# Optimization experiments

Measured on AMD Instinct MI355X. Metric: run time of the kernel, lower is better.

The kernel has to match this reference:

```python
import jax, jax.numpy as jnp
import numpy as np

B, T, NX = 2, 2048, 512
H = 2                    # n_head (structurally forced to 2 by rns() broadcasting)
L = 64                   # num landmarks (cfg.MODEL.LANDMARK)
K = 32                   # rns neighbors per token
HD = NX // H // 2        # differential head dim = 128
EPS = 1e-5


def setup_inputs() -> dict:
    key = jax.random.key(0)
    ks = jax.random.split(key, 16)
    inp = {}
    inp["x"] = jax.random.normal(ks[0], (B, T, NX), jnp.float32)
    # linear weights (torch nn.Linear stores [out,in], applies x @ W.T)
    inp["wq"] = jax.random.normal(ks[1], (NX, NX), jnp.float32) * 0.02
    inp["wk"] = jax.random.normal(ks[2], (NX, NX), jnp.float32) * 0.02
    inp["wv"] = jax.random.normal(ks[3], (NX, NX), jnp.float32) * 0.02
    inp["wo"] = jax.random.normal(ks[4], (NX, NX), jnp.float32) * 0.02
    # landmark modulation params (kaiming-normal-ish init)
    inp["m1"] = jax.random.normal(ks[5], (2 * H, L, 1), jnp.float32)
    inp["m2"] = jax.random.normal(ks[6], (2 * H, 1, L), jnp.float32)
    # differential-attention lambda params
    inp["lq1"] = jax.random.normal(ks[7], (HD,), jnp.float32) * 0.1
    inp["lk1"] = jax.random.normal(ks[8], (HD,), jnp.float32) * 0.1
    inp["lq2"] = jax.random.normal(ks[9], (HD,), jnp.float32) * 0.1
    inp["lk2"] = jax.random.normal(ks[10], (HD,), jnp.float32) * 0.1
    inp["rms_g"] = jnp.ones((2 * HD,), jnp.float32)
    inp["l"] = 3  # layer depth for lambda_init_fn
    inp["num_landmark"] = L
    inp["rns_indices"] = jax.random.randint(ks[11], (B, T, K), 0, T)
    # random.sample(range(t), L) -> distinct indices
    inp["landmark"] = jax.random.permutation(ks[12], T)[:L]
    return inp


def _forward(x, wq, wk, wv, wo, m1, m2, lq1, lk1, lq2, lk2, rms_g,
             l, rns_indices, landmark):
    b, t, nx = x.shape
    hd = nx // H // 2
    q = x @ wq.T
    k = x @ wk.T
    v = x @ wv.T
    qh = q.reshape(b, t, 2 * H, hd).transpose(0, 2, 1, 3)   # [b,2H,t,hd]
    kh = k.reshape(b, t, 2 * H, hd).transpose(0, 2, 3, 1)   # [b,2H,hd,t]
    vh = v.reshape(b, t, H, 2 * hd).transpose(0, 2, 1, 3)   # [b,H,t,2hd]

    # landmark (Nystrom) low-rank factors, L2-normalized over head dim
    sq = qh[:, :, landmark, :]                               # [b,2H,L,hd]
    sk = kh[:, :, :, landmark]                               # [b,2H,hd,L]
    sq = sq / jnp.linalg.norm(sq, axis=3, keepdims=True)
    sk = sk / jnp.linalg.norm(sk, axis=2, keepdims=True)
    sq = m1[None] * sq
    sk = m2[None] * sk

    w1 = jnp.matmul(qh, sk)                                  # [b,2H,t,L]
    w2 = jnp.matmul(sq, kh)                                  # [b,2H,L,t]
    w = jnp.matmul(w1, w2)                                   # [b,2H,t,t]

    lam_init = 0.8 - 0.6 * np.exp(-0.3 * l)
    lam = jnp.exp(jnp.sum(lq1 * lk1)) - jnp.exp(jnp.sum(lq2 * lk2)) + lam_init

    # rns symmetric sparse mask: mask[b,i,j]=1 iff j in rns_indices[b,i] AND i in rns_indices[b,j]
    bi = jnp.arange(b)[:, None, None]
    ti = jnp.arange(t)[None, :, None]
    m = jnp.zeros((b, t, t), x.dtype).at[bi, ti, rns_indices].set(1.0)
    m = m * m.transpose(0, 2, 1)
    m4 = m[:, None]                                          # broadcast over heads

    p = jax.nn.softmax(w * m4 - 1e9 * (1.0 - m4), axis=-1)   # [b,2H,t,t]
    p5 = p.reshape(b, H, 2, t, t)
    # differential mixing (note: second term indexes the HEAD dim, requires H==2)
    wmix = (p5[:, :, 0] - lam * p5[:, :, 1]) + ((1.0 - lam) * p5[:, 1] - p5[:, 0])
    a = jnp.matmul(wmix, vh)                                 # [b,H,t,2hd]

    # RMSNorm sub-layer + (1 - lambda_init) scaling
    a = a * jax.lax.rsqrt(jnp.mean(a * a, axis=-1, keepdims=True) + EPS) * rms_g
    a = a * (1.0 - lam_init)
    return a.transpose(0, 2, 1, 3).reshape(b, t, H * 2 * hd) @ wo.T


def reference(x, wq, wk, wv, wo, m1, m2, lq1, lk1, lq2, lk2, rms_g,
              l, num_landmark, rns_indices, landmark):
    return _forward(x, wq, wk, wv, wo, m1, m2, lq1, lk1, lq2, lk2, rms_g,
                    l, rns_indices, landmark)
```

## Files before the change

### kernel.cpp

```cpp
#include <hip/hip_runtime.h>
#include <hip/hip_bf16.h>

#define BB 2
#define TT 2048
#define NX 512
#define NH 4
#define HD 128
#define LL 64
#define KK 32

typedef __bf16 bf16x8 __attribute__((ext_vector_type(8)));
typedef float f32x4 __attribute__((ext_vector_type(4)));
typedef unsigned short us;
typedef const unsigned int __attribute__((address_space(1)))* gptr_t;
typedef unsigned int __attribute__((address_space(3)))* lptr_t;

__device__ __forceinline__ us f2bf(float f) {
    unsigned u = __float_as_uint(f);
    unsigned r = (u + 0x7fffu + ((u >> 16) & 1u)) >> 16;
    return (us)r;
}
__device__ __forceinline__ float bf2f(us h) {
    return __uint_as_float(((unsigned)h) << 16);
}

__global__ void k_split_all(const float* __restrict__ x,
                            const float* __restrict__ wq, const float* __restrict__ wk,
                            const float* __restrict__ wv, const float* __restrict__ wo,
                            us* __restrict__ x_hi, us* __restrict__ x_lo,
                            us* __restrict__ wqkv_hi, us* __restrict__ wqkv_lo,
                            us* __restrict__ wo_hi, us* __restrict__ wo_lo,
                            const float* __restrict__ lq1, const float* __restrict__ lk1,
                            const float* __restrict__ lq2, const float* __restrict__ lk2,
                            const int* __restrict__ lint, float* __restrict__ scal,
                            float* __restrict__ cs)
{
    const int bidx = blockIdx.x;
    if (bidx == 3072) {
        const int tid = threadIdx.x;
        const f32x4 z = {0.f, 0.f, 0.f, 0.f};
        *reinterpret_cast<f32x4*>(cs + tid * 4) = z;
        if (tid < 64) {
            float s1 = lq1[tid] * lk1[tid] + lq1[tid + 64] * lk1[tid + 64];
            float s2 = lq2[tid] * lk2[tid] + lq2[tid + 64] * lk2[tid + 64];
            for (int off = 32; off; off >>= 1) { s1 += __shfl_xor(s1, off); s2 += __shfl_xor(s2, off); }
            if (tid == 0) {
                float lam_init = 0.8f - 0.6f * expf(-0.3f * (float)lint[0]);
                scal[0] = expf(s1) - expf(s2) + lam_init;
                scal[1] = lam_init;
            }
        }
        return;
    }
    const float* src;
    us* hi;
    us* lo;
    int pos;
    if (bidx < 2048) {
        src = x; hi = x_hi; lo = x_lo;
        pos = bidx * 1024 + threadIdx.x * 4;
    } else {
        const int w = (bidx - 2048) >> 8;
        const int p = (bidx - 2048) & 255;
        pos = p * 1024 + threadIdx.x * 4;
        if (w == 0)      { src = wq; hi = wqkv_hi;          lo = wqkv_lo; }
        else if (w == 1) { src = wk; hi = wqkv_hi + 262144; lo = wqkv_lo + 262144; }
        else if (w == 2) { src = wv; hi = wqkv_hi + 524288; lo = wqkv_lo + 524288; }
        else             { src = wo; hi = wo_hi;            lo = wo_lo; }
    }
    const float4 v = *reinterpret_cast<const float4*>(src + pos);
    ushort4 h, l;
    h.x = f2bf(v.x); l.x = f2bf(v.x - bf2f(h.x));
    h.y = f2bf(v.y); l.y = f2bf(v.y - bf2f(h.y));
    h.z = f2bf(v.z); l.z = f2bf(v.z - bf2f(h.z));
    h.w = f2bf(v.w); l.w = f2bf(v.w - bf2f(h.w));
    *reinterpret_cast<ushort4*>(hi + pos) = h;
    *reinterpret_cast<ushort4*>(lo + pos) = l;
}

template<int BN, int MODE>
__global__ __launch_bounds__(256) void k_gemm_big(
    const us* __restrict__ a_hi, const us* __restrict__ a_lo,
    const us* __restrict__ b_hi, const us* __restrict__ b_lo,
    us* __restrict__ vb, float* __restrict__ cout,
    us* __restrict__ qs_hi, us* __restrict__ qs_lo,
    us* __restrict__ ks_hi, us* __restrict__ ks_lo)
{
    constexpr int NB = BN / 32;
    __shared__ us lsA[64 * 64];
    __shared__ us lsB[BN * 64];
    const int tid = threadIdx.x;
    const int m0 = blockIdx.x * 64, n0 = blockIdx.y * BN;
    const int region = n0 >> 9;
    const int ncol0 = n0 & 511;
    const int l = tid & 63, wid = tid >> 6;
    const int wr = (wid >> 1) * 32, wc = (wid & 1) * (BN / 2);
    const int lr = l & 15;
    const int lkb = (l >> 4) * 16;
    f32x4 acc[2][NB] = {};

    const int r8 = tid >> 3;
    const int swzc8 = (((tid & 7) ^ (r8 & 7)) * 8);

    const int nstep = (MODE == 0) ? (region < 2 ? 24 : 16) : 8;
    for (int kt = 0; kt < nstep; ++kt) {
        const int seg = kt >> 3;
        const int koff = (kt & 7) * 64;
        const us* ab;
        const us* bb;
        if constexpr (MODE == 0) {
            if (region < 2) {
                ab = (seg < 2 ? a_hi : a_lo) + koff + swzc8;
                bb = (seg == 1 ? b_lo : b_hi) + koff + swzc8;
            } else {
                ab = (seg == 0 ? a_hi : a_lo) + koff + swzc8;
                bb = b_hi + koff + swzc8;
            }
        } else {
            ab = a_hi + koff + swzc8;
            bb = b_hi + koff + swzc8;
        }
        #pragma unroll
        for (int j = 0; j < 2; ++j)
            __builtin_amdgcn_global_load_lds((gptr_t)(ab + (size_t)(m0 + j * 32 + r8) * 512),
                                             (lptr_t)(lsA + j * 2048 + tid * 8), 16, 0, 0);
        #pragma unroll
        for (int j = 0; j < BN / 32; ++j)
            __builtin_amdgcn_global_load_lds((gptr_t)(bb + (size_t)(n0 + j * 32 + r8) * 512),
                                             (lptr_t)(lsB + j * 2048 + tid * 8), 16, 0, 0);
        __syncthreads();
        bf16x8 af[2][2], bfr[NB][2];
        #pragma unroll
        for (int m = 0; m < 2; ++m) {
            const int row = wr + m * 16 + lr;
            #pragma unroll
            for (int kk = 0; kk < 2; ++kk) {
                const int cb = (kk * 64 + lkb) ^ ((row & 7) << 4);
                af[m][kk] = *reinterpret_cast<const bf16x8*>(
                    (const char*)lsA + row * 128 + cb);
            }
        }
        #pragma unroll
        for (int n = 0; n < NB; ++n) {
            const int row = wc + n * 16 + lr;
            #pragma unroll
            for (int kk = 0; kk < 2; ++kk) {
                const int cb = (kk * 64 + lkb) ^ ((row & 7) << 4);
                bfr[n][kk] = *reinterpret_cast<const bf16x8*>(
                    (const char*)lsB + row * 128 + cb);
            }
        }
        #pragma unroll
        for (int kk = 0; kk < 2; ++kk)
            #pragma unroll
            for (int m = 0; m < 2; ++m)
                #pragma unroll
                for (int n = 0; n < NB; ++n)
                    acc[m][n] = __builtin_amdgcn_mfma_f32_16x16x32_bf16(
                        af[m][kk], bfr[n][kk], acc[m][n], 0, 0, 0);
        __syncthreads();
    }

    if constexpr (MODE == 0) {
        if (region < 2) {
            us* sh = (region == 0) ? qs_hi : ks_hi;
            us* slo = (region == 0) ? qs_lo : ks_lo;
            #pragma unroll
            for (int m = 0; m < 2; ++m) {
                const int row = m0 + wr + m * 16 + (l >> 4) * 4;
                #pragma unroll
                for (int n = 0; n < NB; ++n) {
                    const int col = ncol0 + wc + n * 16 + lr;
                    #pragma unroll
                    for (int r = 0; r < 4; ++r) {
                        const float val = acc[m][n][r];
                        const us h = f2bf(val);
                        sh[(size_t)(row + r) * 512 + col] = h;
                        slo[(size_t)(row + r) * 512 + col] = f2bf(val - bf2f(h));
                    }
                }
            }
        } else {
            #pragma unroll
            for (int m = 0; m < 2; ++m) {
                const int row = m0 + wr + m * 16 + (l >> 4) * 4;
                #pragma unroll
                for (int n = 0; n < NB; ++n) {
                    const int col = ncol0 + wc + n * 16 + lr;
                    #pragma unroll
                    for (int r = 0; r < 4; ++r)
                        vb[(size_t)(row + r) * 512 + col] = f2bf(acc[m][n][r]);
                }
            }
        }
    } else {
        #pragma unroll
        for (int m = 0; m < 2; ++m) {
            const int row = m0 + wr + m * 16 + (l >> 4) * 4;
            #pragma unroll
            for (int n = 0; n < NB; ++n) {
                const int col = n0 + wc + n * 16 + lr;
                #pragma unroll
                for (int r = 0; r < 4; ++r)
                    cout[(size_t)(row + r) * 512 + col] = acc[m][n][r];
            }
        }
    }
}

__global__ __launch_bounds__(256) void k_w12_colsum(
    const us* __restrict__ q_hi, const us* __restrict__ q_lo,
    const us* __restrict__ k_hi, const us* __restrict__ k_lo,
    const us* __restrict__ kn_hi, const us* __restrict__ kn_lo,
    const us* __restrict__ qn_hi, const us* __restrict__ qn_lo,
    float* __restrict__ w1, float* __restrict__ w2t,
    const us* __restrict__ vb, float* __restrict__ cs)
{
    const int blk = blockIdx.x;
    const int tid = threadIdx.x;
    if (blk >= 384) {
        const int c4 = tid * 4;
        const int b = c4 >> 9, c = c4 & 511;
        const int t0 = (blk - 384) * 64;
        const us* p = vb + ((size_t)(b * TT + t0)) * NX + c;
        f32x4 s = {0.f, 0.f, 0.f, 0.f};
        for (int t = 0; t < 64; ++t) {
            const ushort4 u = *reinterpret_cast<const ushort4*>(p + (size_t)t * NX);
            s[0] += bf2f(u.x); s[1] += bf2f(u.y); s[2] += bf2f(u.z); s[3] += bf2f(u.w);
        }
        atomicAdd(&cs[c4 + 0], s[0]);
        atomicAdd(&cs[c4 + 1], s[1]);
        atomicAdd(&cs[c4 + 2], s[2]);
        atomicAdd(&cs[c4 + 3], s[3]);
        return;
    }
    __shared__ us lsA[64 * 64];
    __shared__ us lsB[64 * 64];
    const int m0 = (blk & 31) * 64;
    const int y = (blk >> 5) % 6;
    const int z = blk / 192;
    const int hh = y % 3, b = y / 3;
    const int h = hh + 1;
    const us* ah = (z ? k_hi : q_hi) + ((size_t)b * 2048) * 512 + h * 128;
    const us* al = (z ? k_lo : q_lo) + ((size_t)b * 2048) * 512 + h * 128;
    const us* bhp = (z ? qn_hi : kn_hi) + (size_t)(b * 4 + h) * 64 * 128;
    const us* blp = (z ? qn_lo : kn_lo) + (size_t)(b * 4 + h) * 64 * 128;
    float* C = (z ? w2t : w1) + (size_t)(b * 3 + hh) * 2048 * 64;

    const int l = tid & 63, wid = tid >> 6;
    const int wr = (wid >> 1) * 32, wc = (wid & 1) * 32;
    const int lr = l & 15;
    const int lkb = (l >> 4) * 16;
    f32x4 acc[2][2] = {};
    const int r8 = tid >> 3;
    const int swzc8 = (((tid & 7) ^ (r8 & 7)) * 8);

    for (int kt = 0; kt < 6; ++kt) {
        const int seg = kt >> 1;
        const int koff = (kt & 1) * 64;
        const us* ab = (seg < 2 ? ah : al) + koff + swzc8;
        const us* bb = (seg == 1 ? blp : bhp) + koff + swzc8;
        #pragma unroll
        for (int j = 0; j < 2; ++j) {
            __builtin_amdgcn_global_load_lds((gptr_t)(ab + (size_t)(m0 + j * 32 + r8) * 512),
                                             (lptr_t)(lsA + j * 2048 + tid * 8), 16, 0, 0);
            __builtin_amdgcn_global_load_lds((gptr_t)(bb + (size_t)(j * 32 + r8) * 128),
                                             (lptr_t)(lsB + j * 2048 + tid * 8), 16, 0, 0);
        }
        __syncthreads();
        bf16x8 af[2][2], bfr[2][2];
        #pragma unroll
        for (int m = 0; m < 2; ++m) {
            const int row = wr + m * 16 + lr;
            #pragma unroll
            for (int kk = 0; kk < 2; ++kk) {
                const int cb = (kk * 64 + lkb) ^ ((row & 7) << 4);
                af[m][kk] = *reinterpret_cast<const bf16x8*>((const char*)lsA + row * 128 + cb);
            }
        }
        #pragma unroll
        for (int n = 0; n < 2; ++n) {
            const int row = wc + n * 16 + lr;
            #pragma unroll
            for (int kk = 0; kk < 2; ++kk) {
                const int cb = (kk * 64 + lkb) ^ ((row & 7) << 4);
                bfr[n][kk] = *reinterpret_cast<const bf16x8*>((const char*)lsB + row * 128 + cb);
            }
        }
        #pragma unroll
        for (int kk = 0; kk < 2; ++kk)
            #pragma unroll
            for (int m = 0; m < 2; ++m)
                #pragma unroll
                for (int n = 0; n < 2; ++n)
                    acc[m][n] = __builtin_amdgcn_mfma_f32_16x16x32_bf16(
                        af[m][kk], bfr[n][kk], acc[m][n], 0, 0, 0);
        __syncthreads();
    }

    #pragma unroll
    for (int m = 0; m < 2; ++m) {
        const int row = m0 + wr + m * 16 + (l >> 4) * 4;
        #pragma unroll
        for (int n = 0; n < 2; ++n) {
            const int col = wc + n * 16 + lr;
            #pragma unroll
            for (int r = 0; r < 4; ++r)
                C[(size_t)(row + r) * 64 + col] = acc[m][n][r];
        }
    }
}

__global__ __launch_bounds__(256) void k_norm_lm(
    const us* __restrict__ q_hi, const us* __restrict__ q_lo,
    const us* __restrict__ k_hi, const us* __restrict__ k_lo,
    const float* __restrict__ m1, const float* __restrict__ m2,
    const int* __restrict__ landmark,
    us* __restrict__ qn_hi, us* __restrict__ qn_lo,
    us* __restrict__ kn_hi, us* __restrict__ kn_lo)
{
    const int idx = blockIdx.x * 4 + (threadIdx.x >> 6);
    const int l = idx & 63;
    const int h = (idx >> 6) & 3;
    const int b = idx >> 8;
    const int lm = landmark[l];
    const int d = threadIdx.x & 63;

    const size_t qoff = ((size_t)(b * TT + lm)) * NX + h * HD;
    const float qa = bf2f(q_hi[qoff + d]) + bf2f(q_lo[qoff + d]);
    const float qb = bf2f(q_hi[qoff + d + 64]) + bf2f(q_lo[qoff + d + 64]);
    const float ka = bf2f(k_hi[qoff + d]) + bf2f(k_lo[qoff + d]);
    const float kb = bf2f(k_hi[qoff + d + 64]) + bf2f(k_lo[qoff + d + 64]);
    float sq = qa * qa + qb * qb;
    float sk = ka * ka + kb * kb;
    for (int off = 32; off; off >>= 1) { sq += __shfl_xor(sq, off); sk += __shfl_xor(sk, off); }
    const float invq = rsqrtf(sq) * m1[h * LL + l];
    const float invk = rsqrtf(sk) * m2[h * LL + l];
    const size_t base = (((size_t)(b * NH + h)) * LL + l) * HD;
    const float vq0 = qa * invq, vq1 = qb * invq;
    const float vk0 = ka * invk, vk1 = kb * invk;
    us h0;
    h0 = f2bf(vq0); qn_hi[base + d] = h0;      qn_lo[base + d] = f2bf(vq0 - bf2f(h0));
    h0 = f2bf(vq1); qn_hi[base + d + 64] = h0; qn_lo[base + d + 64] = f2bf(vq1 - bf2f(h0));
    h0 = f2bf(vk0); kn_hi[base + d] = h0;      kn_lo[base + d] = f2bf(vk0 - bf2f(h0));
    h0 = f2bf(vk1); kn_hi[base + d + 64] = h0; kn_lo[base + d + 64] = f2bf(vk1 - bf2f(h0));
}

__global__ __launch_bounds__(256) void k_sparse_attn(
    const float* __restrict__ w1, const float* __restrict__ w2t,
    const us* __restrict__ vb, const float* __restrict__ cs,
    const int* __restrict__ rns, const float* __restrict__ rms_g,
    const float* __restrict__ scal,
    us* __restrict__ ao)
{
    const int wid = threadIdx.x >> 6;
    const int lane = threadIdx.x & 63;
    const int bi = blockIdx.x * 4 + wid;
    const int b = bi >> 11, i = bi & 2047;

    __shared__ int   sl[4][32];
    __shared__ float plog[4][96];
    __shared__ float wmm[4][2][32];
    __shared__ float w1s[4][3][64];

    const int myidx = lane & 31;
    const int cand = rns[(size_t)bi * KK + myidx];
    int dup = 0;
    #pragma unroll
    for (int kk = 0; kk < 31; ++kk) {
        const int other = __shfl(cand, kk);
        dup |= (kk < myidx) & (other == cand);
    }
    const int* jrow = rns + ((size_t)(b * TT + cand)) * KK + (lane >> 5) * 16;
    int found = 0;
    #pragma unroll
    for (int kk = 0; kk < 16; ++kk) found |= (jrow[kk] == i);
    found |= __shfl_xor(found, 32);
    const int keep = (!dup) && found;
    const unsigned long long mask = __ballot(keep) & 0xffffffffull;
    const int sc = __popcll(mask);
    const int pos = __popcll(mask & ((1ull << myidx) - 1ull));
    if (lane < 32 && keep) sl[wid][pos] = cand;

    const float lam = scal[0], lam_init = scal[1];

    if (sc > 0) {
        #pragma unroll
        for (int r = 0; r < 3; ++r)
            w1s[wid][r][lane] = w1[(((size_t)(b * 3 + r)) * TT + i) * LL + lane];
        const int ntask = 3 * sc;
        for (int t0 = 0; t0 < ntask; t0 += 8) {
            const int t = t0 + (lane >> 3);
            float part = 0.f;
            if (t < ntask) {
                const int hh = t % 3, ss = t / 3;
                const int j = sl[wid][ss];
                const float* w2row = w2t + (((size_t)(b * 3 + hh)) * TT + j) * LL + (lane & 7) * 8;
                const float* w1p = &w1s[wid][hh][(lane & 7) * 8];
                #pragma unroll
                for (int e = 0; e < 8; ++e) part += w1p[e] * w2row[e];
            }
            part += __shfl_xor(part, 1);
            part += __shfl_xor(part, 2);
            part += __shfl_xor(part, 4);
            if (t < ntask && (lane & 7) == 0) plog[wid][t] = part;
        }
        if (lane < 3) {
            float mx = -1e30f;
            for (int ss = 0; ss < sc; ++ss) mx = fmaxf(mx, plog[wid][ss * 3 + lane]);
            float s = 0.f;
            for (int ss = 0; ss < sc; ++ss) {
                const float e = expf(plog[wid][ss * 3 + lane] - mx);
                plog[wid][ss * 3 + lane] = e;
                s += e;
            }
            const float inv = 1.0f / s;
            for (int ss = 0; ss < sc; ++ss) plog[wid][ss * 3 + lane] *= inv;
        }
        if (lane < sc) {
            const float p1 = plog[wid][lane * 3 + 0];
            const float p2 = plog[wid][lane * 3 + 1];
            const float p3 = plog[wid][lane * 3 + 2];
            wmm[wid][0][lane] = (1.0f - lam) * p2 - lam * p1;
            wmm[wid][1][lane] = p2 - p1 + (1.0f - 2.0f * lam) * p3;
        }
    }

    f32x4 acc0 = {0.f, 0.f, 0.f, 0.f}, acc1 = {0.f, 0.f, 0.f, 0.f};
    if (sc == 0) {
        const float cc = (1.0f - 2.0f * lam) * (1.0f / (float)TT);
        const f32x4 c0 = *reinterpret_cast<const f32x4*>(cs + b * NX + lane * 4);
        const f32x4 c1 = *reinterpret_cast<const f32x4*>(cs + b * NX + 256 + lane * 4);
        acc0 = cc * c0;
        acc1 = cc * c1;
    } else {
        for (int ss = 0; ss < sc; ++ss) {
            const float wa = wmm[wid][0][ss], wb = wmm[wid][1][ss];
            const us* vrow = vb + ((size_t)(b * TT + sl[wid][ss])) * NX;
            const ushort4 ua = *reinterpret_cast<const ushort4*>(vrow + lane * 4);
            const ushort4 ub = *reinterpret_cast<const ushort4*>(vrow + 256 + lane * 4);
            acc0[0] += wa * bf2f(ua.x); acc0[1] += wa * bf2f(ua.y);
            acc0[2] += wa * bf2f(ua.z); acc0[3] += wa * bf2f(ua.w);
            acc1[0] += wb * bf2f(ub.x); acc1[1] += wb * bf2f(ub.y);
            acc1[2] += wb * bf2f(ub.z); acc1[3] += wb * bf2f(ub.w);
        }
    }

    float s0 = acc0[0]*acc0[0] + acc0[1]*acc0[1] + acc0[2]*acc0[2] + acc0[3]*acc0[3];
    float s1 = acc1[0]*acc1[0] + acc1[1]*acc1[1] + acc1[2]*acc1[2] + acc1[3]*acc1[3];
    #pragma unroll
    for (int off = 32; off; off >>= 1) { s0 += __shfl_xor(s0, off); s1 += __shfl_xor(s1, off); }
    const float sc0 = rsqrtf(s0 * (1.0f / 256.0f) + 1e-5f);
    const float sc1 = rsqrtf(s1 * (1.0f / 256.0f) + 1e-5f);
    const float og = 1.0f - lam_init;
    const f32x4 g = *reinterpret_cast<const f32x4*>(rms_g + lane * 4);
    ushort4 h0, h1;
    #pragma unroll
    for (int e = 0; e < 4; ++e) {
        (&h0.x)[e] = f2bf(acc0[e] * sc0 * g[e] * og);
        (&h1.x)[e] = f2bf(acc1[e] * sc1 * g[e] * og);
    }
    *reinterpret_cast<ushort4*>(ao + (size_t)bi * NX + lane * 4) = h0;
    *reinterpret_cast<ushort4*>(ao + (size_t)bi * NX + 256 + lane * 4) = h1;
}

extern "C" void kernel_launch(void* const* d_in, const int* in_sizes, int n_in,
                              void* d_out, int out_size, void* d_ws, size_t ws_size,
                              hipStream_t stream)
{
    const float* x    = (const float*)d_in[0];
    const float* wq   = (const float*)d_in[1];
    const float* wk   = (const float*)d_in[2];
    const float* wv   = (const float*)d_in[3];
    const float* wo   = (const float*)d_in[4];
    const float* m1   = (const float*)d_in[5];
    const float* m2   = (const float*)d_in[6];
    const float* lq1  = (const float*)d_in[7];
    const float* lk1  = (const float*)d_in[8];
    const float* lq2  = (const float*)d_in[9];
    const float* lk2  = (const float*)d_in[10];
    const float* rmsg = (const float*)d_in[11];
    const int*   lint = (const int*)d_in[12];
    const int*   rns  = (const int*)d_in[14];
    const int*   lmk  = (const int*)d_in[15];
    float* out = (float*)d_out;
    float* ws  = (float*)d_ws;

    const size_t M2 = 2097152;
    const size_t W3 = 786432;
    float* w1   = ws;
    float* w2t  = ws + W3;
    float* cs   = ws + 2 * W3;
    float* scal = cs + 1024;
    us* S = (us*)(scal + 128);
    us* vb   = S;
    us* x_hi = S + M2;
    us* x_lo = S + 2 * M2;
    us* ao   = x_hi;
    us* q_hi = S + 3 * M2;
    us* q_lo = S + 4 * M2;
    us* k_hi = S + 5 * M2;
    us* k_lo = S + 6 * M2;
    us* wqkv_hi = S + 7 * M2;
    us* wqkv_lo = wqkv_hi + 786432;
    us* wo_hi = wqkv_lo + 786432;
    us* wo_lo = wo_hi + 262144;
    us* qn_hi = wo_lo + 262144;
    us* qn_lo = qn_hi + 65536;
    us* kn_hi = qn_lo + 65536;
    us* kn_lo = kn_hi + 65536;

    k_split_all<<<3073, 256, 0, stream>>>(x, wq, wk, wv, wo,
                                          x_hi, x_lo, wqkv_hi, wqkv_lo, wo_hi, wo_lo,
                                          lq1, lk1, lq2, lk2, lint, scal, cs);

    k_gemm_big<128, 0><<<dim3(64, 12), 256, 0, stream>>>(
        x_hi, x_lo, wqkv_hi, wqkv_lo, vb, nullptr, q_hi, q_lo, k_hi, k_lo);

    k_norm_lm<<<128, 256, 0, stream>>>(q_hi, q_lo, k_hi, k_lo, m1, m2, lmk,
                                       qn_hi, qn_lo, kn_hi, kn_lo);
    k_w12_colsum<<<416, 256, 0, stream>>>(q_hi, q_lo, k_hi, k_lo,
                                          kn_hi, kn_lo, qn_hi, qn_lo, w1, w2t, vb, cs);
    k_sparse_attn<<<1024, 256, 0, stream>>>(w1, w2t, vb, cs, rns, rmsg, scal, ao);

    k_gemm_big<64, 1><<<dim3(64, 8), 256, 0, stream>>>(
        ao, nullptr, wo_hi, nullptr, nullptr, out, nullptr, nullptr, nullptr, nullptr);
}
```

Measured before the change: 140.8 us.

## Precompute neighbor bitmap for mutual-membership test and shrink QKV GEMM tile

Builds a per-row T-bit bitmap of rns neighbors with atomicOr inside extra blocks of the split kernel, so the sparse attention kernel checks mutual membership with one bitmap load instead of scanning 32 indices of each candidate row. This replaces gather-heavy reads with a single word lookup. It adds a memset of the 1 MiB bitmap plus atomic traffic. Separately, the QKV GEMM tile changes from 128 to 64 with twice as many blocks, which raises parallelism.

```diff
diff --git a/kernel.cpp b/kernel.cpp
--- a/kernel.cpp
+++ b/kernel.cpp
@@ -33,9 +33,17 @@
                             const float* __restrict__ lq1, const float* __restrict__ lk1,
                             const float* __restrict__ lq2, const float* __restrict__ lk2,
                             const int* __restrict__ lint, float* __restrict__ scal,
-                            float* __restrict__ cs)
+                            float* __restrict__ cs,
+                            const int* __restrict__ rns, unsigned* __restrict__ bmap)
 {
     const int bidx = blockIdx.x;
+    if (bidx >= 3073) {
+        const int bi = (bidx - 3073) * 8 + (threadIdx.x >> 5);
+        const int lane = threadIdx.x & 31;
+        const int t = rns[(size_t)bi * KK + lane];
+        atomicOr(&bmap[(size_t)bi * 64 + (t >> 5)], 1u << (t & 31));
+        return;
+    }
     if (bidx == 3072) {
         const int tid = threadIdx.x;
         const f32x4 z = {0.f, 0.f, 0.f, 0.f};
@@ -349,8 +357,8 @@
 __global__ __launch_bounds__(256) void k_sparse_attn(
     const float* __restrict__ w1, const float* __restrict__ w2t,
     const us* __restrict__ vb, const float* __restrict__ cs,
-    const int* __restrict__ rns, const float* __restrict__ rms_g,
-    const float* __restrict__ scal,
+    const int* __restrict__ rns, const unsigned* __restrict__ bmap,
+    const float* __restrict__ rms_g, const float* __restrict__ scal,
     us* __restrict__ ao)
 {
     const int wid = threadIdx.x >> 6;
@@ -371,16 +379,12 @@
         const int other = __shfl(cand, kk);
         dup |= (kk < myidx) & (other == cand);
     }
-    const int* jrow = rns + ((size_t)(b * TT + cand)) * KK + (lane >> 5) * 16;
-    int found = 0;
-    #pragma unroll
-    for (int kk = 0; kk < 16; ++kk) found |= (jrow[kk] == i);
-    found |= __shfl_xor(found, 32);
-    const int keep = (!dup) && found;
+    const int found = (bmap[(size_t)(b * TT + cand) * 64 + (i >> 5)] >> (i & 31)) & 1;
+    const int keep = (lane < 32) && (!dup) && found;
     const unsigned long long mask = __ballot(keep) & 0xffffffffull;
     const int sc = __popcll(mask);
     const int pos = __popcll(mask & ((1ull << myidx) - 1ull));
-    if (lane < 32 && keep) sl[wid][pos] = cand;
+    if (keep) sl[wid][pos] = cand;
 
     const float lam = scal[0], lam_init = scal[1];
 
@@ -509,19 +513,22 @@
     us* qn_lo = qn_hi + 65536;
     us* kn_hi = qn_lo + 65536;
     us* kn_lo = kn_hi + 65536;
-
-    k_split_all<<<3073, 256, 0, stream>>>(x, wq, wk, wv, wo,
+    unsigned* bmap = (unsigned*)(kn_lo + 65536);
+
+    hipMemsetAsync(bmap, 0, 262144 * sizeof(unsigned), stream);
+    k_split_all<<<3585, 256, 0, stream>>>(x, wq, wk, wv, wo,
                                           x_hi, x_lo, wqkv_hi, wqkv_lo, wo_hi, wo_lo,
-                                          lq1, lk1, lq2, lk2, lint, scal, cs);
-
-    k_gemm_big<128, 0><<<dim3(64, 12), 256, 0, stream>>>(
+                                          lq1, lk1, lq2, lk2, lint, scal, cs,
+                                          rns, bmap);
+
+    k_gemm_big<64, 0><<<dim3(64, 24), 256, 0, stream>>>(
         x_hi, x_lo, wqkv_hi, wqkv_lo, vb, nullptr, q_hi, q_lo, k_hi, k_lo);
 
     k_norm_lm<<<128, 256, 0, stream>>>(q_hi, q_lo, k_hi, k_lo, m1, m2, lmk,
                                        qn_hi, qn_lo, kn_hi, kn_lo);
     k_w12_colsum<<<416, 256, 0, stream>>>(q_hi, q_lo, k_hi, k_lo,
                                           kn_hi, kn_lo, qn_hi, qn_lo, w1, w2t, vb, cs);
-    k_sparse_attn<<<1024, 256, 0, stream>>>(w1, w2t, vb, cs, rns, rmsg, scal, ao);
+    k_sparse_attn<<<1024, 256, 0, stream>>>(w1, w2t, vb, cs, rns, bmap, rmsg, scal, ao);
 
     k_gemm_big<64, 1><<<dim3(64, 8), 256, 0, stream>>>(
         ao, nullptr, wo_hi, nullptr, nullptr, out, nullptr, nullptr, nullptr, nullptr);
```

New measurement: 147.2 us. +4.6%, slower.
